# Kernel optimization log

Hardware: AMD Instinct MI355X
Metric: run time of the kernel (lower is better)

The kernel has to match this reference:

```python
import jax, jax.numpy as jnp
import numpy as np

N_POINTS = 200000
N_CLUSTS = 2000
PTS_PER_CLUST = 100
N_EDGES = 40000


def setup_inputs() -> dict:
    key = jax.random.key(0)
    k1, k2, k3 = jax.random.split(key, 3)
    data = jax.random.normal(k1, (N_POINTS, 5), dtype=jnp.float32)
    clusts = jax.random.randint(k2, (N_CLUSTS, PTS_PER_CLUST), 0, N_POINTS, dtype=jnp.int64)
    edge_index = jax.random.randint(k3, (2, N_EDGES), 0, N_CLUSTS, dtype=jnp.int64)
    return {"data": data, "clusts": clusts, "edge_index": edge_index}


def reference(data, clusts, edge_index):
    """Fused version of the per-edge gather+cat loop.

    For each edge i=(a,b): rows = data[clusts[a]] ++ data[clusts[b]] (first 5 cols),
    with column 3 overwritten by the edge id i. All edges stacked row-wise.
    """
    E = edge_index.shape[1]
    P = clusts.shape[1]
    # [E, 2, P] point indices for the two clusters of every edge -> [E, 2P]
    idx = clusts[edge_index.T].reshape(E, 2 * P)
    buf = data[idx, :5].astype(jnp.float32)          # [E, 2P, 5]
    edge_id = jnp.arange(E, dtype=buf.dtype)          # stamp edge id into col 3
    buf = buf.at[:, :, 3].set(edge_id[:, None])
    return buf.reshape(E * 2 * P, 5)
```

## Files before the change

### kernel.cpp

```cpp
#include <hip/hip_runtime.h>


#define NPTS_PER_CLUST 100
#define EDGES_PER_BLOCK 4

typedef float f32x4 __attribute__((ext_vector_type(4)));
typedef unsigned short u16x4 __attribute__((ext_vector_type(4)));

static __device__ __forceinline__ unsigned short f2bf_rne(float f) {
    unsigned int u = __float_as_uint(f);
    return (unsigned short)((u + 0x7FFFu + ((u >> 16) & 1u)) >> 16);
}
static __device__ __forceinline__ float bf2f(unsigned short h) {
    return __uint_as_float((unsigned int)h << 16);
}

__global__ __launch_bounds__(256) void compact_kernel(
    const float*    __restrict__ data,
    const int*      __restrict__ clusts,
    unsigned short* __restrict__ compact,
    int nrows)
{
    const int r2 = blockIdx.x * blockDim.x + threadIdx.x;
    const int r0 = r2 * 2;
    if (r0 >= nrows) return;

    const bool has2 = (r0 + 1 < nrows);
    const int p0 = clusts[r0];
    const int p1 = has2 ? clusts[r0 + 1] : p0;

    const f32x4 a  = *reinterpret_cast<const f32x4*>(data + (size_t)p0 * 5);
    const float a4 = data[(size_t)p0 * 5 + 4];
    const f32x4 b  = *reinterpret_cast<const f32x4*>(data + (size_t)p1 * 5);
    const float b4 = data[(size_t)p1 * 5 + 4];

    unsigned short* dst = compact + (size_t)r0 * 5;

    if (has2) {
        u16x4 lo, mid;
        lo[0] = f2bf_rne(a[0]); lo[1] = f2bf_rne(a[1]);
        lo[2] = f2bf_rne(a[2]); lo[3] = f2bf_rne(a[3]);
        mid[0] = f2bf_rne(a4);   mid[1] = f2bf_rne(b[0]);
        mid[2] = f2bf_rne(b[1]); mid[3] = f2bf_rne(b[2]);
        const unsigned int hi =
            (unsigned int)f2bf_rne(b[3]) | ((unsigned int)f2bf_rne(b4) << 16);
        *reinterpret_cast<u16x4*>(dst)     = lo;
        *reinterpret_cast<u16x4*>(dst + 4) = mid;
        *reinterpret_cast<unsigned int*>(dst + 8) = hi;
    } else {
        dst[0] = f2bf_rne(a[0]); dst[1] = f2bf_rne(a[1]);
        dst[2] = f2bf_rne(a[2]); dst[3] = f2bf_rne(a[3]);
        dst[4] = f2bf_rne(a4);
    }
}

__global__ __launch_bounds__(256) void edge_copy_kernel(
    const int*            __restrict__ edge_index,
    const unsigned short* __restrict__ compact,
    float*                __restrict__ out,
    int E)
{
    __shared__ int sh_cl[2 * EDGES_PER_BLOCK];

    const int b = blockIdx.x;
    const int t = threadIdx.x;
    const int e0 = b * EDGES_PER_BLOCK;
    const int n_e = min(EDGES_PER_BLOCK, E - e0);
    const int n_f4 = n_e * 250;

    if (t < 2 * EDGES_PER_BLOCK) {
        const int el   = t >> 1;
        const int half = t & 1;
        sh_cl[t] = (el < n_e) ? edge_index[half * E + (e0 + el)] : 0;
    }
    __syncthreads();

    u16x4 hv[4];
    int   ki[4];
    int   el_a[4];

#pragma unroll
    for (int k = 0; k < 4; ++k) {
        const int i = t + k * 256;
        if (i < n_f4) {
            const int el   = i / 250;
            const int q    = i - el * 250;
            const int half = (q >= 125);
            const int qq   = q - half * 125;
            const int cl   = sh_cl[el * 2 + half];
            hv[k] = reinterpret_cast<const u16x4*>(compact + (size_t)cl * 500)[qq];
            const int m = (q * 4) % 5;
            ki[k]   = (3 - m + 5) % 5;
            el_a[k] = el;
        }
    }

#pragma unroll
    for (int k = 0; k < 4; ++k) {
        const int i = t + k * 256;
        if (i < n_f4) {
            f32x4 v;
            v[0] = bf2f(hv[k][0]);
            v[1] = bf2f(hv[k][1]);
            v[2] = bf2f(hv[k][2]);
            v[3] = bf2f(hv[k][3]);
            const float ef = (float)(e0 + el_a[k]);
            const int kk = ki[k];
            if      (kk == 0) v[0] = ef;
            else if (kk == 1) v[1] = ef;
            else if (kk == 2) v[2] = ef;
            else if (kk == 3) v[3] = ef;
            __builtin_nontemporal_store(v,
                reinterpret_cast<f32x4*>(out + (size_t)b * (EDGES_PER_BLOCK * 1000)) + i);
        }
    }
}

__global__ __launch_bounds__(256) void direct_kernel(
    const float* __restrict__ data,
    const int*   __restrict__ clusts,
    const int*   __restrict__ edge_index,
    float*       __restrict__ out,
    int E)
{
    __shared__ int sh_pts[2 * NPTS_PER_CLUST];
    const int e = blockIdx.x;
    const int t = threadIdx.x;
    if (t < 2 * NPTS_PER_CLUST) {
        const int cl  = (t < NPTS_PER_CLUST) ? edge_index[e] : edge_index[E + e];
        const int off = (t < NPTS_PER_CLUST) ? t : t - NPTS_PER_CLUST;
        sh_pts[t] = clusts[cl * NPTS_PER_CLUST + off];
    }
    __syncthreads();
    if (t < 250) {
        const float edge_f = (float)e;
        float vals[4];
#pragma unroll
        for (int kk = 0; kk < 4; ++kk) {
            const int el = t * 4 + kk;
            const int r  = el / 5;
            const int cc = el - r * 5;
            vals[kk] = (cc == 3) ? edge_f : data[sh_pts[r] * 5 + cc];
        }
        float4 w; w.x = vals[0]; w.y = vals[1]; w.z = vals[2]; w.w = vals[3];
        reinterpret_cast<float4*>(out + (size_t)e * 1000)[t] = w;
    }
}

extern "C" void kernel_launch(void* const* d_in, const int* in_sizes, int n_in,
                              void* d_out, int out_size, void* d_ws, size_t ws_size,
                              hipStream_t stream) {
    const float* data       = (const float*)d_in[0];
    const int*   clusts     = (const int*)d_in[1];
    const int*   edge_index = (const int*)d_in[2];
    float*       out        = (float*)d_out;

    const int E        = in_sizes[2] / 2;
    const int nrows    = in_sizes[1];
    const int total    = nrows * 5;
    const size_t need  = (size_t)total * sizeof(unsigned short);

    if (ws_size >= need) {
        unsigned short* compact = (unsigned short*)d_ws;
        const int npairs = (nrows + 1) / 2;
        compact_kernel<<<(npairs + 255) / 256, 256, 0, stream>>>(data, clusts, compact, nrows);
        const int nblk = (E + EDGES_PER_BLOCK - 1) / EDGES_PER_BLOCK;
        edge_copy_kernel<<<nblk, 256, 0, stream>>>(edge_index, compact, out, E);
    } else {
        direct_kernel<<<E, 256, 0, stream>>>(data, clusts, edge_index, out, E);
    }
}
```

Measured before the change: 41.01 us.

## Fuse compaction and edge copy into one cooperative persistent kernel

```diff
diff --git a/kernel.cpp b/kernel.cpp
--- a/kernel.cpp
+++ b/kernel.cpp
@@ -1,4 +1,7 @@
 #include <hip/hip_runtime.h>
+#include <hip/hip_cooperative_groups.h>
+
+namespace cg = cooperative_groups;
 
 
 #define NPTS_PER_CLUST 100
@@ -15,16 +18,13 @@
     return __uint_as_float((unsigned int)h << 16);
 }
 
-__global__ __launch_bounds__(256) void compact_kernel(
-    const float*    __restrict__ data,
-    const int*      __restrict__ clusts,
-    unsigned short* __restrict__ compact,
-    int nrows)
-{
-    const int r2 = blockIdx.x * blockDim.x + threadIdx.x;
-    const int r0 = r2 * 2;
+
+static __device__ __forceinline__ void compact_pair(
+    const float* __restrict__ data, const int* __restrict__ clusts,
+    unsigned short* __restrict__ compact, int pr, int nrows)
+{
+    const int r0 = pr * 2;
     if (r0 >= nrows) return;
-
     const bool has2 = (r0 + 1 < nrows);
     const int p0 = clusts[r0];
     const int p1 = has2 ? clusts[r0 + 1] : p0;
@@ -35,7 +35,6 @@
     const float b4 = data[(size_t)p1 * 5 + 4];
 
     unsigned short* dst = compact + (size_t)r0 * 5;
-
     if (has2) {
         u16x4 lo, mid;
         lo[0] = f2bf_rne(a[0]); lo[1] = f2bf_rne(a[1]);
@@ -54,16 +53,10 @@
     }
 }
 
-__global__ __launch_bounds__(256) void edge_copy_kernel(
-    const int*            __restrict__ edge_index,
-    const unsigned short* __restrict__ compact,
-    float*                __restrict__ out,
-    int E)
-{
-    __shared__ int sh_cl[2 * EDGES_PER_BLOCK];
-
-    const int b = blockIdx.x;
-    const int t = threadIdx.x;
+static __device__ __forceinline__ void edge_quad(
+    const int* __restrict__ edge_index, const unsigned short* __restrict__ compact,
+    float* __restrict__ out, int E, int b, int t, int* sh_cl)
+{
     const int e0 = b * EDGES_PER_BLOCK;
     const int n_e = min(EDGES_PER_BLOCK, E - e0);
     const int n_f4 = n_e * 250;
@@ -116,12 +109,51 @@
     }
 }
 
+
+__global__ __launch_bounds__(256) void fused_kernel(
+    const float* __restrict__ data, const int* __restrict__ clusts,
+    const int* __restrict__ edge_index, float* __restrict__ out,
+    unsigned short* __restrict__ compact, int E, int nrows)
+{
+    __shared__ int sh_cl[2 * EDGES_PER_BLOCK];
+    const int t   = threadIdx.x;
+    const int tid = blockIdx.x * blockDim.x + t;
+    const int nthr = gridDim.x * blockDim.x;
+
+    const int npairs = (nrows + 1) / 2;
+    for (int pr = tid; pr < npairs; pr += nthr)
+        compact_pair(data, clusts, compact, pr, nrows);
+
+    cg::this_grid().sync();
+
+    const int nquads = (E + EDGES_PER_BLOCK - 1) / EDGES_PER_BLOCK;
+    for (int b = blockIdx.x; b < nquads; b += gridDim.x) {
+        edge_quad(edge_index, compact, out, E, b, t, sh_cl);
+        __syncthreads();
+    }
+}
+
+
+__global__ __launch_bounds__(256) void compact_kernel(
+    const float* __restrict__ data, const int* __restrict__ clusts,
+    unsigned short* __restrict__ compact, int nrows)
+{
+    const int pr = blockIdx.x * blockDim.x + threadIdx.x;
+    compact_pair(data, clusts, compact, pr, nrows);
+}
+
+__global__ __launch_bounds__(256) void edge_copy_kernel(
+    const int* __restrict__ edge_index, const unsigned short* __restrict__ compact,
+    float* __restrict__ out, int E)
+{
+    __shared__ int sh_cl[2 * EDGES_PER_BLOCK];
+    edge_quad(edge_index, compact, out, E, blockIdx.x, threadIdx.x, sh_cl);
+}
+
+
 __global__ __launch_bounds__(256) void direct_kernel(
-    const float* __restrict__ data,
-    const int*   __restrict__ clusts,
-    const int*   __restrict__ edge_index,
-    float*       __restrict__ out,
-    int E)
+    const float* __restrict__ data, const int* __restrict__ clusts,
+    const int* __restrict__ edge_index, float* __restrict__ out, int E)
 {
     __shared__ int sh_pts[2 * NPTS_PER_CLUST];
     const int e = blockIdx.x;
@@ -155,18 +187,33 @@
     const int*   edge_index = (const int*)d_in[2];
     float*       out        = (float*)d_out;
 
-    const int E        = in_sizes[2] / 2;
-    const int nrows    = in_sizes[1];
-    const int total    = nrows * 5;
-    const size_t need  = (size_t)total * sizeof(unsigned short);
-
-    if (ws_size >= need) {
-        unsigned short* compact = (unsigned short*)d_ws;
-        const int npairs = (nrows + 1) / 2;
-        compact_kernel<<<(npairs + 255) / 256, 256, 0, stream>>>(data, clusts, compact, nrows);
-        const int nblk = (E + EDGES_PER_BLOCK - 1) / EDGES_PER_BLOCK;
-        edge_copy_kernel<<<nblk, 256, 0, stream>>>(edge_index, compact, out, E);
-    } else {
+    const int E     = in_sizes[2] / 2;
+    const int nrows = in_sizes[1];
+    const size_t need = (size_t)nrows * 5 * sizeof(unsigned short);
+
+    if (ws_size < need) {
         direct_kernel<<<E, 256, 0, stream>>>(data, clusts, edge_index, out, E);
-    }
-}
+        return;
+    }
+
+    unsigned short* compact = (unsigned short*)d_ws;
+    int e_arg = E, nr_arg = nrows;
+
+    int occ = 0;
+    hipError_t st = hipOccupancyMaxActiveBlocksPerMultiprocessor(
+        &occ, (const void*)fused_kernel, 256, 0);
+    if (st == hipSuccess && occ > 0) {
+        int blocks = occ * 256;
+        if (blocks > 2048) blocks = 2048;
+        void* args[] = {(void*)&data, (void*)&clusts, (void*)&edge_index,
+                        (void*)&out, (void*)&compact, (void*)&e_arg, (void*)&nr_arg};
+        st = hipLaunchCooperativeKernel((const void*)fused_kernel,
+                                        dim3(blocks), dim3(256), args, 0, stream);
+        if (st == hipSuccess) return;
+    }
+
+    const int npairs = (nrows + 1) / 2;
+    compact_kernel<<<(npairs + 255) / 256, 256, 0, stream>>>(data, clusts, compact, nrows);
+    const int nblk = (E + EDGES_PER_BLOCK - 1) / EDGES_PER_BLOCK;
+    edge_copy_kernel<<<nblk, 256, 0, stream>>>(edge_index, compact, out, E);
+}
```

Result: slower. 131.8 us (+221.4%).
